# Kernel tuning notes

Measured on AMD Instinct MI355X. Metric: run time of the kernel, lower is better.

The kernel has to match this reference:

```python
import jax, jax.numpy as jnp
import numpy as np

N = 524288      # number of evaluation points (particles)
NMODE = 8       # number of eikonal modes
NCOEF = 6       # Gauss-Hermite coefficients per mode (full h00..h02 branch)
NFIELD = 2      # fields: (phi, A_parallel)
NPSI = 512      # psi interpolation grid size
K = 3           # alpha branches from the Clebsch mapping (2*pi shifts)
R0 = 1.7        # major radius for the theta stand-in mapping
DX = 1.0 / (NPSI - 1)
TWO_PI = 2.0 * np.pi


def cubic_interp(xq, table):
    """Catmull-Rom cubic interpolation on a uniform grid over [0, 1].
    xq: [N]; table: [NPSI] or [NPSI, Nmode]. Returns [N] or [N, Nmode]."""
    npts = table.shape[0]
    s = xq / jnp.asarray(DX, xq.dtype)
    i = jnp.clip(jnp.floor(s).astype(jnp.int32), 1, npts - 3)
    tt = s - i.astype(xq.dtype)
    tt = tt.reshape(tt.shape + (1,) * (table.ndim - 1))  # broadcast over trailing dims
    fm1, f0, f1, f2 = table[i - 1], table[i], table[i + 1], table[i + 2]
    t2 = tt * tt
    t3 = t2 * tt
    wm1 = 0.5 * (-t3 + 2.0 * t2 - tt)
    w0 = 0.5 * (3.0 * t3 - 5.0 * t2 + 2.0)
    w1 = 0.5 * (-3.0 * t3 + 4.0 * t2 + tt)
    w2 = 0.5 * (t3 - t2)
    return wm1 * fm1 + w0 * f0 + w1 * f1 + w2 * f2


def _hermite_poly(c, x, y, h20, h11, h02):
    """c: [M, 6, F] (real or imag part); x: [N, M]; y/h11/h02: [N, M, K].
    Returns p: [N, M, K, F] = sum_j c_j * H_j(x, y)."""
    return (c[None, :, None, 0, :]
            + c[:, 1, :][None, :, None, :] * x[:, :, None, None]
            + c[:, 2, :][None, :, None, :] * y[..., None]
            + c[:, 3, :][None, :, None, :] * h20[:, :, None, None]
            + c[:, 4, :][None, :, None, :] * h11[..., None]
            + c[:, 5, :][None, :, None, :] * h02[..., None])


def _forward(t, r, varphi, z, psi, gh_re, gh_im, alpha0_table, iota_table,
             psi0, psi_scale, alpha_scale, omega, n):
    theta = jnp.arctan2(z, r - R0)                                   # [N]
    iota = cubic_interp(psi, iota_table)                             # [N]
    alpha0 = cubic_interp(psi, alpha0_table)                         # [N, M]
    shifts = jnp.asarray([-TWO_PI, 0.0, TWO_PI], dtype=psi.dtype)    # [K]
    alpha = iota[:, None] * (theta[:, None] + shifts[None, :])       # [N, K]

    x = (psi[:, None] - psi0) / psi_scale                            # [N, M]
    y = (alpha[:, None, :] - alpha0[:, :, None]) / alpha_scale[None, :, None]  # [N, M, K]
    g = jnp.exp(-0.5 * (jnp.square(x)[..., None] + jnp.square(y)))   # [N, M, K]

    h20 = 4.0 * jnp.square(x) - 2.0                                  # [N, M]
    h11 = x[..., None] * y                                           # [N, M, K]
    h02 = 4.0 * jnp.square(y) - 2.0                                  # [N, M, K]

    p_re = _hermite_poly(gh_re, x, y, h20, h11, h02)                 # [N, M, K, F]
    p_im = _hermite_poly(gh_im, x, y, h20, h11, h02)                 # [N, M, K, F]

    nf = n.astype(psi.dtype)
    phase = (omega[None, :, None] * t
             - nf[None, :, None] * (varphi[:, None, None]
                                    - (alpha[:, None, :] - alpha0[:, :, None])))  # [N, M, K]

    ev = (jnp.einsum('nmkf,nmk->nf', p_re, g * jnp.cos(phase))
          - jnp.einsum('nmkf,nmk->nf', p_im, g * jnp.sin(phase)))    # [N, F]
    return ev


def setup_inputs() -> dict:
    key = jax.random.key(0)
    ks = jax.random.split(key, 14)
    t = jax.random.uniform(ks[0], (), jnp.float32) * 10.0
    r = R0 + (jax.random.uniform(ks[1], (N,), jnp.float32) - 0.5)          # around major radius
    varphi = jax.random.uniform(ks[2], (N,), jnp.float32) * TWO_PI
    z = (jax.random.uniform(ks[3], (N,), jnp.float32) - 0.5)
    psi = 0.05 + 0.9 * jax.random.uniform(ks[4], (N,), jnp.float32)        # stay interior to grid
    gh_re = jax.random.normal(ks[5], (NMODE, NCOEF, NFIELD), jnp.float32) * 0.5
    gh_im = jax.random.normal(ks[6], (NMODE, NCOEF, NFIELD), jnp.float32) * 0.5
    alpha0_table = jax.random.normal(ks[7], (NPSI, NMODE), jnp.float32) * 0.1
    iota_table = 1.0 + 0.5 * jax.random.uniform(ks[8], (NPSI,), jnp.float32)
    psi0 = 0.2 + 0.6 * jax.random.uniform(ks[9], (NMODE,), jnp.float32)
    psi_scale = 0.05 + 0.1 * jax.random.uniform(ks[10], (NMODE,), jnp.float32)
    alpha_scale = 0.4 + 0.4 * jax.random.uniform(ks[11], (NMODE,), jnp.float32)
    omega = jax.random.normal(ks[12], (NMODE,), jnp.float32)
    n = jax.random.randint(ks[13], (NMODE,), 1, 20, jnp.int32)
    return {"t": t, "r": r, "varphi": varphi, "z": z, "psi": psi,
            "gh_re": gh_re, "gh_im": gh_im, "alpha0_table": alpha0_table,
            "iota_table": iota_table, "psi0": psi0, "psi_scale": psi_scale,
            "alpha_scale": alpha_scale, "omega": omega, "n": n}


def reference(t, r, varphi, z, psi, gh_re, gh_im, alpha0_table, iota_table,
              psi0, psi_scale, alpha_scale, omega, n):
    return _forward(t, r, varphi, z, psi, gh_re, gh_im, alpha0_table,
                    iota_table, psi0, psi_scale, alpha_scale, omega, n)
```

## Files before the change

### kernel.cpp

```cpp
#include <hip/hip_runtime.h>

#define NMODE 8
#define NPSI  512

__global__ void eik_kernel(
    const float* __restrict__ t_p,
    const float* __restrict__ r_p,
    const float* __restrict__ vp_p,
    const float* __restrict__ z_p,
    const float* __restrict__ psi_p,
    const float* __restrict__ ghre_p,
    const float* __restrict__ ghim_p,
    const float* __restrict__ a0tab_p,
    const float* __restrict__ iotatab_p,
    const float* __restrict__ psi0_p,
    const float* __restrict__ psisc_p,
    const float* __restrict__ alsc_p,
    const float* __restrict__ omega_p,
    const int*   __restrict__ nmode_p,
    float* __restrict__ out,
    int npart)
{
    constexpr float R0      = 1.7f;
    constexpr float TWO_PI  = 6.28318530717958647692f;
    constexpr float INV_2PI = 0.15915494309189533577f;
    constexpr float NHL2E   = -0.72134752044448170368f;

    __shared__ float s_iota[NPSI];
    __shared__ float s_a0[NMODE][NPSI];
    __shared__ float s_md[NMODE][32];

    const int tid = threadIdx.x;

    for (int p = tid; p < NPSI; p += 256) s_iota[p] = iotatab_p[p];
    for (int idx = tid; idx < NPSI * NMODE; idx += 256) {
        s_a0[idx & 7][idx >> 3] = a0tab_p[idx];
    }
    if (tid < NMODE * 12) {
        int m = tid / 12, j = tid - m * 12;
        s_md[m][j]      = ghre_p[m * 12 + j];
        s_md[m][12 + j] = ghim_p[m * 12 + j];
    }
    if (tid < NMODE) {
        s_md[tid][24] = psi0_p[tid];
        s_md[tid][25] = 1.0f / psisc_p[tid];
        s_md[tid][26] = 1.0f / alsc_p[tid];
        s_md[tid][27] = omega_p[tid] * t_p[0];
        s_md[tid][28] = (float)nmode_p[tid];
    }
    __syncthreads();

    const int i = blockIdx.x * 256 + tid;
    if (i >= npart) return;

    const float ps = psi_p[i];
    const float rr = r_p[i];
    const float zz = z_p[i];
    const float vp = vp_p[i];

    const float theta = atan2f(zz, rr - R0);

    const float s = ps * (float)(NPSI - 1);
    int ii = (int)floorf(s);
    ii = ii < 1 ? 1 : (ii > NPSI - 3 ? NPSI - 3 : ii);
    const float tt = s - (float)ii;
    const float t2 = tt * tt, t3 = t2 * tt;
    const float wm1 = 0.5f * (-t3 + 2.0f * t2 - tt);
    const float w0  = 0.5f * (3.0f * t3 - 5.0f * t2 + 2.0f);
    const float w1  = 0.5f * (-3.0f * t3 + 4.0f * t2 + tt);
    const float w2  = 0.5f * (t3 - t2);

    const float iota = wm1 * s_iota[ii - 1] + w0 * s_iota[ii]
                     + w1 * s_iota[ii + 1] + w2 * s_iota[ii + 2];
    const float at      = iota * theta;
    const float dy_base = iota * TWO_PI;

    float acc0 = 0.0f, acc1 = 0.0f;

    for (int m = 0; m < NMODE; ++m) {
        const float* md = s_md[m];
        const float a0 = wm1 * s_a0[m][ii - 1] + w0 * s_a0[m][ii]
                       + w1 * s_a0[m][ii + 1] + w2 * s_a0[m][ii + 2];
        const float x      = (ps - md[24]) * md[25];
        const float inv_as = md[26];
        const float ot     = md[27];
        const float nf     = md[28];

        const float xx    = x * x;
        const float h20   = 4.0f * xx - 2.0f;
        const float xterm = xx * NHL2E;
        const float base  = at - a0;
        const float y1    = base * inv_as;
        const float dy    = dy_base * inv_as;
        const float pcr = (ot - nf * (vp - base)) * INV_2PI;
        const float dpr = nf * iota;

        const float pxr0 = md[0]  + md[2]  * x + md[6]  * h20;
        const float pxr1 = md[1]  + md[3]  * x + md[7]  * h20;
        const float pxi0 = md[12] + md[14] * x + md[18] * h20;
        const float pxi1 = md[13] + md[15] * x + md[19] * h20;

        #pragma unroll
        for (int k = 0; k < 3; ++k) {
            const float kf  = (float)(k - 1);
            const float y   = fmaf(kf, dy,  y1);
            const float phr = fmaf(kf, dpr, pcr);
            const float yy  = y * y;
            const float g   = __builtin_amdgcn_exp2f(fmaf(yy, NHL2E, xterm));
            const float fr  = __builtin_amdgcn_fractf(phr);
            const float sn  = __builtin_amdgcn_sinf(fr);
            const float cs  = __builtin_amdgcn_cosf(fr);
            const float h11 = x * y;
            const float h02 = fmaf(4.0f, yy, -2.0f);

            const float pr0 = pxr0 + md[4]  * y + md[8]  * h11 + md[10] * h02;
            const float pr1 = pxr1 + md[5]  * y + md[9]  * h11 + md[11] * h02;
            const float pi0 = pxi0 + md[16] * y + md[20] * h11 + md[22] * h02;
            const float pi1 = pxi1 + md[17] * y + md[21] * h11 + md[23] * h02;

            const float gc = g * cs;
            const float gs = g * sn;
            acc0 = fmaf(pr0, gc, acc0);
            acc0 = fmaf(pi0, -gs, acc0);
            acc1 = fmaf(pr1, gc, acc1);
            acc1 = fmaf(pi1, -gs, acc1);
        }
    }

    reinterpret_cast<float2*>(out)[i] = make_float2(acc0, acc1);
}

extern "C" void kernel_launch(void* const* d_in, const int* in_sizes, int n_in,
                              void* d_out, int out_size, void* d_ws, size_t ws_size,
                              hipStream_t stream) {
    const float* t      = (const float*)d_in[0];
    const float* r      = (const float*)d_in[1];
    const float* varphi = (const float*)d_in[2];
    const float* z      = (const float*)d_in[3];
    const float* psi    = (const float*)d_in[4];
    const float* gh_re  = (const float*)d_in[5];
    const float* gh_im  = (const float*)d_in[6];
    const float* a0t    = (const float*)d_in[7];
    const float* iot    = (const float*)d_in[8];
    const float* psi0   = (const float*)d_in[9];
    const float* psc    = (const float*)d_in[10];
    const float* asc    = (const float*)d_in[11];
    const float* omg    = (const float*)d_in[12];
    const int*   nn     = (const int*)d_in[13];
    float* out = (float*)d_out;

    const int npart  = in_sizes[1];
    const int blocks = (npart + 255) / 256;
    eik_kernel<<<blocks, 256, 0, stream>>>(t, r, varphi, z, psi, gh_re, gh_im,
                                           a0t, iot, psi0, psc, asc, omg, nn,
                                           out, npart);
}
```

Baseline: 113.3 us.

## Process two particles per thread and read mode coefficients as uniform scalars

Each thread now evaluates two particles (i and i+N/2), which halves the grid and spreads the per-block shared-memory table fill over twice as much work. Per-mode coefficients now come from global memory as wave-uniform scalar loads instead of shared memory, and the Hermite polynomial is refactored so the x-dependent parts of the y coefficient are hoisted out of the k loop. The costs are higher register pressure and fewer waves to hide latency, and an odd npart would leave its last particle unprocessed.

```diff
diff --git a/kernel.cpp b/kernel.cpp
--- a/kernel.cpp
+++ b/kernel.cpp
@@ -3,7 +3,7 @@
 #define NMODE 8
 #define NPSI  512
 
-__global__ void eik_kernel(
+__global__ __launch_bounds__(256) void eik_kernel(
     const float* __restrict__ t_p,
     const float* __restrict__ r_p,
     const float* __restrict__ vp_p,
@@ -28,106 +28,172 @@
 
     __shared__ float s_iota[NPSI];
     __shared__ float s_a0[NMODE][NPSI];
-    __shared__ float s_md[NMODE][32];
 
     const int tid = threadIdx.x;
-
     for (int p = tid; p < NPSI; p += 256) s_iota[p] = iotatab_p[p];
-    for (int idx = tid; idx < NPSI * NMODE; idx += 256) {
+    for (int idx = tid; idx < NPSI * NMODE; idx += 256)
         s_a0[idx & 7][idx >> 3] = a0tab_p[idx];
-    }
-    if (tid < NMODE * 12) {
-        int m = tid / 12, j = tid - m * 12;
-        s_md[m][j]      = ghre_p[m * 12 + j];
-        s_md[m][12 + j] = ghim_p[m * 12 + j];
-    }
-    if (tid < NMODE) {
-        s_md[tid][24] = psi0_p[tid];
-        s_md[tid][25] = 1.0f / psisc_p[tid];
-        s_md[tid][26] = 1.0f / alsc_p[tid];
-        s_md[tid][27] = omega_p[tid] * t_p[0];
-        s_md[tid][28] = (float)nmode_p[tid];
-    }
     __syncthreads();
 
-    const int i = blockIdx.x * 256 + tid;
-    if (i >= npart) return;
-
-    const float ps = psi_p[i];
-    const float rr = r_p[i];
-    const float zz = z_p[i];
-    const float vp = vp_p[i];
-
-    const float theta = atan2f(zz, rr - R0);
-
-    const float s = ps * (float)(NPSI - 1);
-    int ii = (int)floorf(s);
-    ii = ii < 1 ? 1 : (ii > NPSI - 3 ? NPSI - 3 : ii);
-    const float tt = s - (float)ii;
-    const float t2 = tt * tt, t3 = t2 * tt;
-    const float wm1 = 0.5f * (-t3 + 2.0f * t2 - tt);
-    const float w0  = 0.5f * (3.0f * t3 - 5.0f * t2 + 2.0f);
-    const float w1  = 0.5f * (-3.0f * t3 + 4.0f * t2 + tt);
-    const float w2  = 0.5f * (t3 - t2);
-
-    const float iota = wm1 * s_iota[ii - 1] + w0 * s_iota[ii]
-                     + w1 * s_iota[ii + 1] + w2 * s_iota[ii + 2];
-    const float at      = iota * theta;
-    const float dy_base = iota * TWO_PI;
-
-    float acc0 = 0.0f, acc1 = 0.0f;
+    const int half = npart >> 1;
+    const int i0 = blockIdx.x * 256 + tid;
+    if (i0 >= half) return;
+    const int i1 = i0 + half;
+
+    const float tval = t_p[0];
+
+    const float psA = psi_p[i0];
+    const float psB = psi_p[i1];
+    const float thA = atan2f(z_p[i0], r_p[i0] - R0);
+    const float thB = atan2f(z_p[i1], r_p[i1] - R0);
+    const float vpA = vp_p[i0];
+    const float vpB = vp_p[i1];
+
+    float sA = psA * (float)(NPSI - 1);
+    int iiA = (int)floorf(sA);
+    iiA = iiA < 1 ? 1 : (iiA > NPSI - 3 ? NPSI - 3 : iiA);
+    const float ttA = sA - (float)iiA;
+    const float tA2 = ttA * ttA, tA3 = tA2 * ttA;
+    const float wAm1 = 0.5f * (-tA3 + 2.0f * tA2 - ttA);
+    const float wA0  = 0.5f * (3.0f * tA3 - 5.0f * tA2 + 2.0f);
+    const float wA1  = 0.5f * (-3.0f * tA3 + 4.0f * tA2 + ttA);
+    const float wA2  = 0.5f * (tA3 - tA2);
+
+    float sB = psB * (float)(NPSI - 1);
+    int iiB = (int)floorf(sB);
+    iiB = iiB < 1 ? 1 : (iiB > NPSI - 3 ? NPSI - 3 : iiB);
+    const float ttB = sB - (float)iiB;
+    const float tB2 = ttB * ttB, tB3 = tB2 * ttB;
+    const float wBm1 = 0.5f * (-tB3 + 2.0f * tB2 - ttB);
+    const float wB0  = 0.5f * (3.0f * tB3 - 5.0f * tB2 + 2.0f);
+    const float wB1  = 0.5f * (-3.0f * tB3 + 4.0f * tB2 + ttB);
+    const float wB2  = 0.5f * (tB3 - tB2);
+
+    const float iotaA = wAm1 * s_iota[iiA - 1] + wA0 * s_iota[iiA]
+                      + wA1 * s_iota[iiA + 1] + wA2 * s_iota[iiA + 2];
+    const float iotaB = wBm1 * s_iota[iiB - 1] + wB0 * s_iota[iiB]
+                      + wB1 * s_iota[iiB + 1] + wB2 * s_iota[iiB + 2];
+
+    const float atA  = iotaA * thA;
+    const float atB  = iotaB * thB;
+    const float dybA = iotaA * TWO_PI;
+    const float dybB = iotaB * TWO_PI;
+
+    float acc00 = 0.0f, acc01 = 0.0f;
+    float acc10 = 0.0f, acc11 = 0.0f;
 
     for (int m = 0; m < NMODE; ++m) {
-        const float* md = s_md[m];
-        const float a0 = wm1 * s_a0[m][ii - 1] + w0 * s_a0[m][ii]
-                       + w1 * s_a0[m][ii + 1] + w2 * s_a0[m][ii + 2];
-        const float x      = (ps - md[24]) * md[25];
-        const float inv_as = md[26];
-        const float ot     = md[27];
-        const float nf     = md[28];
-
-        const float xx    = x * x;
-        const float h20   = 4.0f * xx - 2.0f;
-        const float xterm = xx * NHL2E;
-        const float base  = at - a0;
-        const float y1    = base * inv_as;
-        const float dy    = dy_base * inv_as;
-        const float pcr = (ot - nf * (vp - base)) * INV_2PI;
-        const float dpr = nf * iota;
-
-        const float pxr0 = md[0]  + md[2]  * x + md[6]  * h20;
-        const float pxr1 = md[1]  + md[3]  * x + md[7]  * h20;
-        const float pxi0 = md[12] + md[14] * x + md[18] * h20;
-        const float pxi1 = md[13] + md[15] * x + md[19] * h20;
-
-        #pragma unroll
-        for (int k = 0; k < 3; ++k) {
-            const float kf  = (float)(k - 1);
-            const float y   = fmaf(kf, dy,  y1);
-            const float phr = fmaf(kf, dpr, pcr);
-            const float yy  = y * y;
-            const float g   = __builtin_amdgcn_exp2f(fmaf(yy, NHL2E, xterm));
-            const float fr  = __builtin_amdgcn_fractf(phr);
-            const float sn  = __builtin_amdgcn_sinf(fr);
-            const float cs  = __builtin_amdgcn_cosf(fr);
-            const float h11 = x * y;
-            const float h02 = fmaf(4.0f, yy, -2.0f);
-
-            const float pr0 = pxr0 + md[4]  * y + md[8]  * h11 + md[10] * h02;
-            const float pr1 = pxr1 + md[5]  * y + md[9]  * h11 + md[11] * h02;
-            const float pi0 = pxi0 + md[16] * y + md[20] * h11 + md[22] * h02;
-            const float pi1 = pxi1 + md[17] * y + md[21] * h11 + md[23] * h02;
-
-            const float gc = g * cs;
-            const float gs = g * sn;
-            acc0 = fmaf(pr0, gc, acc0);
-            acc0 = fmaf(pi0, -gs, acc0);
-            acc1 = fmaf(pr1, gc, acc1);
-            acc1 = fmaf(pi1, -gs, acc1);
+        const float c0r0 = ghre_p[m*12+ 0], c0r1 = ghre_p[m*12+ 1];
+        const float c1r0 = ghre_p[m*12+ 2], c1r1 = ghre_p[m*12+ 3];
+        const float c2r0 = ghre_p[m*12+ 4], c2r1 = ghre_p[m*12+ 5];
+        const float c3r0 = ghre_p[m*12+ 6], c3r1 = ghre_p[m*12+ 7];
+        const float c4r0 = ghre_p[m*12+ 8], c4r1 = ghre_p[m*12+ 9];
+        const float c5r0 = ghre_p[m*12+10], c5r1 = ghre_p[m*12+11];
+        const float c0i0 = ghim_p[m*12+ 0], c0i1 = ghim_p[m*12+ 1];
+        const float c1i0 = ghim_p[m*12+ 2], c1i1 = ghim_p[m*12+ 3];
+        const float c2i0 = ghim_p[m*12+ 4], c2i1 = ghim_p[m*12+ 5];
+        const float c3i0 = ghim_p[m*12+ 6], c3i1 = ghim_p[m*12+ 7];
+        const float c4i0 = ghim_p[m*12+ 8], c4i1 = ghim_p[m*12+ 9];
+        const float c5i0 = ghim_p[m*12+10], c5i1 = ghim_p[m*12+11];
+        const float psi0m = psi0_p[m];
+        const float ipsc  = __builtin_amdgcn_rcpf(psisc_p[m]);
+        const float iasc  = __builtin_amdgcn_rcpf(alsc_p[m]);
+        const float ot    = omega_p[m] * tval;
+        const float nf    = (float)nmode_p[m];
+
+        const float* row = s_a0[m];
+
+        {
+            const float a0 = wAm1 * row[iiA - 1] + wA0 * row[iiA]
+                           + wA1 * row[iiA + 1] + wA2 * row[iiA + 2];
+            const float x     = (psA - psi0m) * ipsc;
+            const float xx    = x * x;
+            const float h20   = fmaf(4.0f, xx, -2.0f);
+            const float xterm = xx * NHL2E;
+            const float base  = atA - a0;
+            const float y1    = base * iasc;
+            const float dy    = dybA * iasc;
+            const float pcr   = (ot - nf * (vpA - base)) * INV_2PI;
+            const float dpr   = nf * iotaA;
+
+            const float pxr0 = fmaf(c3r0, h20, fmaf(c1r0, x, c0r0));
+            const float pxr1 = fmaf(c3r1, h20, fmaf(c1r1, x, c0r1));
+            const float pxi0 = fmaf(c3i0, h20, fmaf(c1i0, x, c0i0));
+            const float pxi1 = fmaf(c3i1, h20, fmaf(c1i1, x, c0i1));
+            const float er0  = fmaf(c4r0, x, c2r0);
+            const float er1  = fmaf(c4r1, x, c2r1);
+            const float ei0  = fmaf(c4i0, x, c2i0);
+            const float ei1  = fmaf(c4i1, x, c2i1);
+
+            #pragma unroll
+            for (int k = 0; k < 3; ++k) {
+                const float kf  = (float)(k - 1);
+                const float y   = fmaf(kf, dy, y1);
+                const float phr = fmaf(kf, dpr, pcr);
+                const float yy  = y * y;
+                const float g   = __builtin_amdgcn_exp2f(fmaf(yy, NHL2E, xterm));
+                const float fr  = __builtin_amdgcn_fractf(phr);
+                const float sn  = __builtin_amdgcn_sinf(fr);
+                const float cs  = __builtin_amdgcn_cosf(fr);
+                const float h02 = fmaf(4.0f, yy, -2.0f);
+                const float pr0 = fmaf(c5r0, h02, fmaf(er0, y, pxr0));
+                const float pr1 = fmaf(c5r1, h02, fmaf(er1, y, pxr1));
+                const float pi0 = fmaf(c5i0, h02, fmaf(ei0, y, pxi0));
+                const float pi1 = fmaf(c5i1, h02, fmaf(ei1, y, pxi1));
+                const float gc = g * cs;
+                const float gs = g * sn;
+                acc00 = fmaf(pr0, gc, acc00); acc00 = fmaf(pi0, -gs, acc00);
+                acc01 = fmaf(pr1, gc, acc01); acc01 = fmaf(pi1, -gs, acc01);
+            }
+        }
+
+        {
+            const float a0 = wBm1 * row[iiB - 1] + wB0 * row[iiB]
+                           + wB1 * row[iiB + 1] + wB2 * row[iiB + 2];
+            const float x     = (psB - psi0m) * ipsc;
+            const float xx    = x * x;
+            const float h20   = fmaf(4.0f, xx, -2.0f);
+            const float xterm = xx * NHL2E;
+            const float base  = atB - a0;
+            const float y1    = base * iasc;
+            const float dy    = dybB * iasc;
+            const float pcr   = (ot - nf * (vpB - base)) * INV_2PI;
+            const float dpr   = nf * iotaB;
+
+            const float pxr0 = fmaf(c3r0, h20, fmaf(c1r0, x, c0r0));
+            const float pxr1 = fmaf(c3r1, h20, fmaf(c1r1, x, c0r1));
+            const float pxi0 = fmaf(c3i0, h20, fmaf(c1i0, x, c0i0));
+            const float pxi1 = fmaf(c3i1, h20, fmaf(c1i1, x, c0i1));
+            const float er0  = fmaf(c4r0, x, c2r0);
+            const float er1  = fmaf(c4r1, x, c2r1);
+            const float ei0  = fmaf(c4i0, x, c2i0);
+            const float ei1  = fmaf(c4i1, x, c2i1);
+
+            #pragma unroll
+            for (int k = 0; k < 3; ++k) {
+                const float kf  = (float)(k - 1);
+                const float y   = fmaf(kf, dy, y1);
+                const float phr = fmaf(kf, dpr, pcr);
+                const float yy  = y * y;
+                const float g   = __builtin_amdgcn_exp2f(fmaf(yy, NHL2E, xterm));
+                const float fr  = __builtin_amdgcn_fractf(phr);
+                const float sn  = __builtin_amdgcn_sinf(fr);
+                const float cs  = __builtin_amdgcn_cosf(fr);
+                const float h02 = fmaf(4.0f, yy, -2.0f);
+                const float pr0 = fmaf(c5r0, h02, fmaf(er0, y, pxr0));
+                const float pr1 = fmaf(c5r1, h02, fmaf(er1, y, pxr1));
+                const float pi0 = fmaf(c5i0, h02, fmaf(ei0, y, pxi0));
+                const float pi1 = fmaf(c5i1, h02, fmaf(ei1, y, pxi1));
+                const float gc = g * cs;
+                const float gs = g * sn;
+                acc10 = fmaf(pr0, gc, acc10); acc10 = fmaf(pi0, -gs, acc10);
+                acc11 = fmaf(pr1, gc, acc11); acc11 = fmaf(pi1, -gs, acc11);
+            }
         }
     }
 
-    reinterpret_cast<float2*>(out)[i] = make_float2(acc0, acc1);
+    reinterpret_cast<float2*>(out)[i0] = make_float2(acc00, acc01);
+    reinterpret_cast<float2*>(out)[i1] = make_float2(acc10, acc11);
 }
 
 extern "C" void kernel_launch(void* const* d_in, const int* in_sizes, int n_in,
@@ -149,8 +215,9 @@
     const int*   nn     = (const int*)d_in[13];
     float* out = (float*)d_out;
 
-    const int npart  = in_sizes[1];
-    const int blocks = (npart + 255) / 256;
+    const int npart = in_sizes[1];
+    const int half  = npart >> 1;
+    const int blocks = (half + 255) / 256;
     eik_kernel<<<blocks, 256, 0, stream>>>(t, r, varphi, z, psi, gh_re, gh_im,
                                            a0t, iot, psi0, psc, asc, omg, nn,
                                            out, npart);
```

After: 99.18 us. 12.5% less time.

## Pack psi tables into one interleaved shared array, read mode params as uniform globals

Applied to the files above, without the earlier changes.

Interleaves the alpha0 and iota tables into a single row-major shared array with stride 12. Each thread then does the 4-point cubic interpolation for all modes using vectorized float4 LDS reads, and the table is filled with vector global loads. Per-mode coefficients now come straight from global memory as uniform (scalar) loads instead of a shared staging array, and particle loads and atan2 are issued before the barrier. The mode loop is fully unrolled, the Hermite terms are refactored into fewer FMAs, and launch bounds are added; together these raise register pressure.

```diff
diff --git a/kernel.cpp b/kernel.cpp
--- a/kernel.cpp
+++ b/kernel.cpp
@@ -1,9 +1,10 @@
 #include <hip/hip_runtime.h>
 
-#define NMODE 8
-#define NPSI  512
+#define NMODE   8
+#define NPSI    512
+#define RSTRIDE 12
 
-__global__ void eik_kernel(
+__global__ __launch_bounds__(256, 4) void eik_kernel(
     const float* __restrict__ t_p,
     const float* __restrict__ r_p,
     const float* __restrict__ vp_p,
@@ -26,104 +27,132 @@
     constexpr float INV_2PI = 0.15915494309189533577f;
     constexpr float NHL2E   = -0.72134752044448170368f;
 
-    __shared__ float s_iota[NPSI];
-    __shared__ float s_a0[NMODE][NPSI];
-    __shared__ float s_md[NMODE][32];
+    __shared__ float s_pack[NPSI][RSTRIDE];
 
     const int tid = threadIdx.x;
+    const int i   = blockIdx.x * 256 + tid;
+    const bool live = (i < npart);
 
-    for (int p = tid; p < NPSI; p += 256) s_iota[p] = iotatab_p[p];
-    for (int idx = tid; idx < NPSI * NMODE; idx += 256) {
-        s_a0[idx & 7][idx >> 3] = a0tab_p[idx];
+    float ps = 0.f, th = 0.f, vp = 0.f;
+    if (live) {
+        ps = psi_p[i];
+        th = atan2f(z_p[i], r_p[i] - R0);
+        vp = vp_p[i];
     }
-    if (tid < NMODE * 12) {
-        int m = tid / 12, j = tid - m * 12;
-        s_md[m][j]      = ghre_p[m * 12 + j];
-        s_md[m][12 + j] = ghim_p[m * 12 + j];
-    }
-    if (tid < NMODE) {
-        s_md[tid][24] = psi0_p[tid];
-        s_md[tid][25] = 1.0f / psisc_p[tid];
-        s_md[tid][26] = 1.0f / alsc_p[tid];
-        s_md[tid][27] = omega_p[tid] * t_p[0];
-        s_md[tid][28] = (float)nmode_p[tid];
-    }
-    __syncthreads();
-
-    const int i = blockIdx.x * 256 + tid;
-    if (i >= npart) return;
-
-    const float ps = psi_p[i];
-    const float rr = r_p[i];
-    const float zz = z_p[i];
-    const float vp = vp_p[i];
-
-    const float theta = atan2f(zz, rr - R0);
 
     const float s = ps * (float)(NPSI - 1);
     int ii = (int)floorf(s);
     ii = ii < 1 ? 1 : (ii > NPSI - 3 ? NPSI - 3 : ii);
     const float tt = s - (float)ii;
     const float t2 = tt * tt, t3 = t2 * tt;
-    const float wm1 = 0.5f * (-t3 + 2.0f * t2 - tt);
-    const float w0  = 0.5f * (3.0f * t3 - 5.0f * t2 + 2.0f);
-    const float w1  = 0.5f * (-3.0f * t3 + 4.0f * t2 + tt);
-    const float w2  = 0.5f * (t3 - t2);
+    float w[4];
+    w[0] = 0.5f * (-t3 + 2.0f * t2 - tt);
+    w[1] = 0.5f * (3.0f * t3 - 5.0f * t2 + 2.0f);
+    w[2] = 0.5f * (-3.0f * t3 + 4.0f * t2 + tt);
+    w[3] = 0.5f * (t3 - t2);
 
-    const float iota = wm1 * s_iota[ii - 1] + w0 * s_iota[ii]
-                     + w1 * s_iota[ii + 1] + w2 * s_iota[ii + 2];
-    const float at      = iota * theta;
-    const float dy_base = iota * TWO_PI;
+    for (int p = tid; p < NPSI; p += 256) {
+        const float4* src = reinterpret_cast<const float4*>(a0tab_p + p * 8);
+        const float4 lo = src[0];
+        const float4 hi = src[1];
+        const float  io = iotatab_p[p];
+        float* dst = s_pack[p];
+        *reinterpret_cast<float4*>(dst)     = lo;
+        *reinterpret_cast<float4*>(dst + 4) = hi;
+        dst[8] = io;
+    }
+    __syncthreads();
+
+    if (!live) return;
+
+    float a0v[NMODE];
+    #pragma unroll
+    for (int q = 0; q < NMODE; ++q) a0v[q] = 0.0f;
+    float iotv = 0.0f;
+
+    #pragma unroll
+    for (int j = 0; j < 4; ++j) {
+        const float* rowp = s_pack[ii - 1 + j];
+        const float4 lo = *reinterpret_cast<const float4*>(rowp);
+        const float4 hi = *reinterpret_cast<const float4*>(rowp + 4);
+        const float  io = rowp[8];
+        const float  wj = w[j];
+        a0v[0] = fmaf(wj, lo.x, a0v[0]);
+        a0v[1] = fmaf(wj, lo.y, a0v[1]);
+        a0v[2] = fmaf(wj, lo.z, a0v[2]);
+        a0v[3] = fmaf(wj, lo.w, a0v[3]);
+        a0v[4] = fmaf(wj, hi.x, a0v[4]);
+        a0v[5] = fmaf(wj, hi.y, a0v[5]);
+        a0v[6] = fmaf(wj, hi.z, a0v[6]);
+        a0v[7] = fmaf(wj, hi.w, a0v[7]);
+        iotv   = fmaf(wj, io,   iotv);
+    }
+
+    const float tval = t_p[0];
+    const float at   = iotv * th;
+    const float dyb  = iotv * TWO_PI;
 
     float acc0 = 0.0f, acc1 = 0.0f;
 
+    #pragma unroll
     for (int m = 0; m < NMODE; ++m) {
-        const float* md = s_md[m];
-        const float a0 = wm1 * s_a0[m][ii - 1] + w0 * s_a0[m][ii]
-                       + w1 * s_a0[m][ii + 1] + w2 * s_a0[m][ii + 2];
-        const float x      = (ps - md[24]) * md[25];
-        const float inv_as = md[26];
-        const float ot     = md[27];
-        const float nf     = md[28];
+        const float c0r0 = ghre_p[m*12+ 0], c0r1 = ghre_p[m*12+ 1];
+        const float c1r0 = ghre_p[m*12+ 2], c1r1 = ghre_p[m*12+ 3];
+        const float c2r0 = ghre_p[m*12+ 4], c2r1 = ghre_p[m*12+ 5];
+        const float c3r0 = ghre_p[m*12+ 6], c3r1 = ghre_p[m*12+ 7];
+        const float c4r0 = ghre_p[m*12+ 8], c4r1 = ghre_p[m*12+ 9];
+        const float c5r0 = ghre_p[m*12+10], c5r1 = ghre_p[m*12+11];
+        const float c0i0 = ghim_p[m*12+ 0], c0i1 = ghim_p[m*12+ 1];
+        const float c1i0 = ghim_p[m*12+ 2], c1i1 = ghim_p[m*12+ 3];
+        const float c2i0 = ghim_p[m*12+ 4], c2i1 = ghim_p[m*12+ 5];
+        const float c3i0 = ghim_p[m*12+ 6], c3i1 = ghim_p[m*12+ 7];
+        const float c4i0 = ghim_p[m*12+ 8], c4i1 = ghim_p[m*12+ 9];
+        const float c5i0 = ghim_p[m*12+10], c5i1 = ghim_p[m*12+11];
+        const float psi0m = psi0_p[m];
+        const float ipsc  = __builtin_amdgcn_rcpf(psisc_p[m]);
+        const float iasc  = __builtin_amdgcn_rcpf(alsc_p[m]);
+        const float ot    = omega_p[m] * tval;
+        const float nf    = (float)nmode_p[m];
 
+        const float a0    = a0v[m];
+        const float x     = (ps - psi0m) * ipsc;
         const float xx    = x * x;
-        const float h20   = 4.0f * xx - 2.0f;
+        const float h20   = fmaf(4.0f, xx, -2.0f);
         const float xterm = xx * NHL2E;
         const float base  = at - a0;
-        const float y1    = base * inv_as;
-        const float dy    = dy_base * inv_as;
-        const float pcr = (ot - nf * (vp - base)) * INV_2PI;
-        const float dpr = nf * iota;
+        const float y1    = base * iasc;
+        const float dy    = dyb * iasc;
+        const float pcr   = (ot - nf * (vp - base)) * INV_2PI;
+        const float dpr   = nf * iotv;
 
-        const float pxr0 = md[0]  + md[2]  * x + md[6]  * h20;
-        const float pxr1 = md[1]  + md[3]  * x + md[7]  * h20;
-        const float pxi0 = md[12] + md[14] * x + md[18] * h20;
-        const float pxi1 = md[13] + md[15] * x + md[19] * h20;
+        const float pxr0 = fmaf(c3r0, h20, fmaf(c1r0, x, c0r0));
+        const float pxr1 = fmaf(c3r1, h20, fmaf(c1r1, x, c0r1));
+        const float pxi0 = fmaf(c3i0, h20, fmaf(c1i0, x, c0i0));
+        const float pxi1 = fmaf(c3i1, h20, fmaf(c1i1, x, c0i1));
+        const float er0  = fmaf(c4r0, x, c2r0);
+        const float er1  = fmaf(c4r1, x, c2r1);
+        const float ei0  = fmaf(c4i0, x, c2i0);
+        const float ei1  = fmaf(c4i1, x, c2i1);
 
         #pragma unroll
         for (int k = 0; k < 3; ++k) {
             const float kf  = (float)(k - 1);
-            const float y   = fmaf(kf, dy,  y1);
+            const float y   = fmaf(kf, dy, y1);
             const float phr = fmaf(kf, dpr, pcr);
             const float yy  = y * y;
             const float g   = __builtin_amdgcn_exp2f(fmaf(yy, NHL2E, xterm));
             const float fr  = __builtin_amdgcn_fractf(phr);
             const float sn  = __builtin_amdgcn_sinf(fr);
             const float cs  = __builtin_amdgcn_cosf(fr);
-            const float h11 = x * y;
             const float h02 = fmaf(4.0f, yy, -2.0f);
-
-            const float pr0 = pxr0 + md[4]  * y + md[8]  * h11 + md[10] * h02;
-            const float pr1 = pxr1 + md[5]  * y + md[9]  * h11 + md[11] * h02;
-            const float pi0 = pxi0 + md[16] * y + md[20] * h11 + md[22] * h02;
-            const float pi1 = pxi1 + md[17] * y + md[21] * h11 + md[23] * h02;
-
+            const float pr0 = fmaf(c5r0, h02, fmaf(er0, y, pxr0));
+            const float pr1 = fmaf(c5r1, h02, fmaf(er1, y, pxr1));
+            const float pi0 = fmaf(c5i0, h02, fmaf(ei0, y, pxi0));
+            const float pi1 = fmaf(c5i1, h02, fmaf(ei1, y, pxi1));
             const float gc = g * cs;
             const float gs = g * sn;
-            acc0 = fmaf(pr0, gc, acc0);
-            acc0 = fmaf(pi0, -gs, acc0);
-            acc1 = fmaf(pr1, gc, acc1);
-            acc1 = fmaf(pi1, -gs, acc1);
+            acc0 = fmaf(pr0, gc, acc0); acc0 = fmaf(pi0, -gs, acc0);
+            acc1 = fmaf(pr1, gc, acc1); acc1 = fmaf(pi1, -gs, acc1);
         }
     }
 
```

After: 96.88 us. 1.17x faster.
